# Kernel tuning notes

Measured on AMD Instinct MI355X. Metric: run time of the kernel, lower is better.

The kernel has to match this reference:

```python
import jax, jax.numpy as jnp
import numpy as np

IN_DIM = 96
HIDDEN = 256
EPS = 1e-6
NEG = -1e10


def setup_inputs() -> dict:
    key = jax.random.key(0)
    ks = jax.random.split(key, 12)
    B, S = 8, 2048
    q = jax.random.normal(ks[0], (B, S, IN_DIM), dtype=jnp.float32)
    k = jax.random.normal(ks[1], (B, S, IN_DIM), dtype=jnp.float32)
    v = jax.random.normal(ks[2], (B, S, IN_DIM), dtype=jnp.float32)
    mask = jax.random.randint(ks[3], (B, S, S), 0, 2, dtype=jnp.int32)
    s = 1.0 / np.sqrt(IN_DIM)
    Wq = jax.random.normal(ks[4], (IN_DIM, HIDDEN), dtype=jnp.float32) * s
    bq = jax.random.normal(ks[5], (HIDDEN,), dtype=jnp.float32) * 0.01
    Wk = jax.random.normal(ks[6], (IN_DIM, HIDDEN), dtype=jnp.float32) * s
    bk = jax.random.normal(ks[7], (HIDDEN,), dtype=jnp.float32) * 0.01
    Wv = jax.random.normal(ks[8], (IN_DIM, HIDDEN), dtype=jnp.float32) * s
    bv = jax.random.normal(ks[9], (HIDDEN,), dtype=jnp.float32) * 0.01
    gamma = jnp.ones((HIDDEN,), dtype=jnp.float32)
    beta = jnp.zeros((HIDDEN,), dtype=jnp.float32)
    return {"query": q, "key": k, "value": v, "mask": mask,
            "Wq": Wq, "bq": bq, "Wk": Wk, "bk": bk, "Wv": Wv, "bv": bv,
            "gamma": gamma, "beta": beta}


def reference(query, key, value, mask, Wq, bq, Wk, bk, Wv, bv, gamma, beta):
    # Linear projections: [B,S,96] @ [96,H] -> [B,S,H]
    q = jnp.einsum('bsf,fh->bsh', query, Wq) + bq
    k = jnp.einsum('bsf,fh->bsh', key, Wk) + bk
    v = jnp.einsum('bsf,fh->bsh', value, Wv) + bv
    # Scaled dot-product scores: [B,S,S]
    score = jnp.einsum('bqh,bkh->bqk', q, k) / jnp.sqrt(jnp.float32(HIDDEN))
    score = jnp.where(mask == 0, jnp.float32(NEG), score)
    attn = jax.nn.softmax(score, axis=-1)
    out = jnp.einsum('bqk,bkh->bqh', attn, v)
    # LayerNorm over last dim, eps=1e-6
    mu = jnp.mean(out, axis=-1, keepdims=True)
    var = jnp.mean(jnp.square(out - mu), axis=-1, keepdims=True)
    normed = (out - mu) * jax.lax.rsqrt(var + EPS)
    return normed * gamma + beta
```

## Files before the change

### kernel.cpp

```cpp
#include <hip/hip_runtime.h>

#define B_   8
#define S_   2048
#define IN_  96
#define H_   256
#define NROW (B_ * S_)

typedef float    f32x4 __attribute__((ext_vector_type(4)));
typedef _Float16 f16x8 __attribute__((ext_vector_type(8)));
typedef int      i32x4 __attribute__((ext_vector_type(4)));

__device__ __forceinline__ unsigned short f2h(float x) {
    return __builtin_bit_cast(unsigned short, (_Float16)x);
}
__device__ __forceinline__ float h2f(unsigned short x) {
    return (float)__builtin_bit_cast(_Float16, x);
}
__device__ __forceinline__ void lds_barrier() {
    asm volatile("s_waitcnt lgkmcnt(0)\n\ts_barrier" ::: "memory");
}

__global__ __launch_bounds__(256) void wconv_kernel(
    const float* __restrict__ Wq, const float* __restrict__ Wk,
    const float* __restrict__ Wv, unsigned short* __restrict__ wt)
{
    const int p  = blockIdx.x >> 3;
    const int h0 = (blockIdx.x & 7) * 32;
    const float* W = (p == 0) ? Wq : (p == 1) ? Wk : Wv;
    unsigned short* dst = wt + (size_t)p * H_ * IN_ + (size_t)h0 * IN_;

    __shared__ unsigned short lds[32][100];
    const int t = threadIdx.x;
    #pragma unroll
    for (int i = 0; i < 12; ++i) {
        int idx = i * 256 + t;
        int f = idx >> 5;
        int hl = idx & 31;
        lds[hl][f] = f2h(W[f * H_ + h0 + hl]);
    }
    __syncthreads();
    #pragma unroll
    for (int j = 0; j < 6; ++j) {
        int e = (j * 256 + t) * 2;
        int hl = e / IN_, f = e % IN_;
        unsigned int pk = (unsigned int)lds[hl][f] |
                          ((unsigned int)lds[hl][f + 1] << 16);
        ((unsigned int*)dst)[j * 256 + t] = pk;
    }
}

__global__ __launch_bounds__(256) void projmask_kernel(
    const float* __restrict__ query, const float* __restrict__ key,
    const float* __restrict__ value, const unsigned short* __restrict__ wt,
    const float* __restrict__ bq, const float* __restrict__ bk,
    const float* __restrict__ bv, const int* __restrict__ mask,
    unsigned short* __restrict__ pq, unsigned short* __restrict__ pk,
    unsigned short* __restrict__ pv, unsigned* __restrict__ pm32)
{
    __shared__ unsigned short Xs[3][16][104];
    __shared__ unsigned char nib[4][8][64];

    const int bid = blockIdx.x;
    if ((bid % 3) == 2) {
        const int wave = threadIdx.x >> 6;
        const int lane = threadIdx.x & 63;
        const int wid  = (bid / 3) * 4 + wave;
        #pragma unroll
        for (int rr = 0; rr < 4; ++rr) {
            const int r0 = wid * 8 + rr * 2;
            const int* m0 = mask + (size_t)r0 * S_ + lane * 4;
            const int* m1 = m0 + S_;
            i32x4 a[8], b[8];
            #pragma unroll
            for (int j = 0; j < 8; ++j)
                a[j] = __builtin_nontemporal_load((const i32x4*)(m0 + j * 256));
            #pragma unroll
            for (int j = 0; j < 8; ++j)
                b[j] = __builtin_nontemporal_load((const i32x4*)(m1 + j * 256));

            #pragma unroll
            for (int j = 0; j < 8; ++j) {
                unsigned n0 = (a[j][0] != 0 ? 1u : 0u) | (a[j][1] != 0 ? 2u : 0u)
                            | (a[j][2] != 0 ? 4u : 0u) | (a[j][3] != 0 ? 8u : 0u);
                unsigned n1 = (b[j][0] != 0 ? 1u : 0u) | (b[j][1] != 0 ? 2u : 0u)
                            | (b[j][2] != 0 ? 4u : 0u) | (b[j][3] != 0 ? 8u : 0u);
                nib[wave][j][lane] = (unsigned char)(n0 | (n1 << 4));
            }
            asm volatile("s_waitcnt lgkmcnt(0)" ::: "memory");

            unsigned long long v = *(const unsigned long long*)
                &nib[wave][lane >> 3][(lane & 7) * 8];
            unsigned long long x0 = v & 0x0F0F0F0F0F0F0F0FULL;
            unsigned long long x1 = (v >> 4) & 0x0F0F0F0F0F0F0F0FULL;
            x0 = (x0 | (x0 >> 4))  & 0x00FF00FF00FF00FFULL;
            x1 = (x1 | (x1 >> 4))  & 0x00FF00FF00FF00FFULL;
            x0 = (x0 | (x0 >> 8))  & 0x0000FFFF0000FFFFULL;
            x1 = (x1 | (x1 >> 8))  & 0x0000FFFF0000FFFFULL;
            x0 = (x0 | (x0 >> 16)) & 0xFFFFFFFFULL;
            x1 = (x1 | (x1 >> 16)) & 0xFFFFFFFFULL;

            pm32[(size_t)r0 * 64 + lane]       = (unsigned)x0;
            pm32[(size_t)(r0 + 1) * 64 + lane] = (unsigned)x1;
        }
        return;
    }
    const int bi = (bid / 3) * 2 + (bid % 3);

    const int t    = threadIdx.x;
    const int lane = t & 63;
    const int wave = t >> 6;
    const int col  = lane & 15;
    const int quad = lane >> 4;
    const int s0   = bi * 16;
    const int b    = s0 >> 11;
    const int sl   = s0 & (S_ - 1);

    const float* srcs[3] = { query + (size_t)s0 * IN_,
                             key   + (size_t)s0 * IN_,
                             value + (size_t)s0 * IN_ };
    #pragma unroll
    for (int p = 0; p < 3; ++p) {
        #pragma unroll
        for (int i = 0; i < 2; ++i) {
            int idx = i * 256 + t;
            if (idx < 384) {
                f32x4 x = *(const f32x4*)(srcs[p] + idx * 4);
                int r = idx / 24;
                int f = (idx - r * 24) * 4;
                unsigned long long pkk =
                    (unsigned long long)f2h(x[0])
                  | ((unsigned long long)f2h(x[1]) << 16)
                  | ((unsigned long long)f2h(x[2]) << 32)
                  | ((unsigned long long)f2h(x[3]) << 48);
                *(unsigned long long*)&Xs[p][r][f] = pkk;
            }
        }
    }
    __syncthreads();

    const int hc = wave;
    #pragma unroll
    for (int p = 0; p < 3; ++p) {
        const unsigned short* wbase = wt + (size_t)p * H_ * IN_;
        f16x8 wfr[4][3];
        #pragma unroll
        for (int ht = 0; ht < 4; ++ht)
            #pragma unroll
            for (int kc = 0; kc < 3; ++kc)
                wfr[ht][kc] = *(const f16x8*)(wbase
                    + (size_t)(hc * 64 + ht * 16 + col) * IN_ + kc * 32 + quad * 8);
        f16x8 xfr[3];
        #pragma unroll
        for (int kc = 0; kc < 3; ++kc)
            xfr[kc] = *(const f16x8*)&Xs[p][col][kc * 32 + quad * 8];

        f32x4 acc[4];
        #pragma unroll
        for (int ht = 0; ht < 4; ++ht) acc[ht] = (f32x4)(0.0f);
        #pragma unroll
        for (int kc = 0; kc < 3; ++kc)
            #pragma unroll
            for (int ht = 0; ht < 4; ++ht)
                acc[ht] = (p < 2)
                    ? __builtin_amdgcn_mfma_f32_16x16x32_f16(xfr[kc], wfr[ht][kc], acc[ht], 0, 0, 0)
                    : __builtin_amdgcn_mfma_f32_16x16x32_f16(wfr[ht][kc], xfr[kc], acc[ht], 0, 0, 0);

        if (p < 2) {
            unsigned short* dst  = (p == 0) ? pq : pk;
            const float*    bias = (p == 0) ? bq : bk;
            #pragma unroll
            for (int ht = 0; ht < 4; ++ht) {
                float bh = bias[hc * 64 + ht * 16 + col];
                const int s    = hc * 2 + (ht >> 1);
                const int lq   = ((ht & 1) * 2 + (col >> 3)) * 16;
                const int j    = col & 7;
                #pragma unroll
                for (int r = 0; r < 4; ++r)
                    dst[(size_t)(((bi * 8 + s) * 64 + lq + quad * 4 + r)) * 8 + j]
                        = f2h(acc[ht][r] + bh);
            }
        } else {
            const int kl  = (sl & 63) + col;
            const int c   = sl >> 6;
            const int s2  = kl >> 5;
            const int qv  = (kl >> 3) & 3;
            const int jj  = col & 7;
            #pragma unroll
            for (int ht = 0; ht < 4; ++ht) {
                f32x4 b4 = *(const f32x4*)(bv + hc * 64 + ht * 16 + quad * 4);
                #pragma unroll
                for (int r = 0; r < 4; ++r)
                    pv[(size_t)(((b * 32 + c) * 32 + hc * 8 + ht * 2 + s2) * 64
                                + qv * 16 + quad * 4 + r) * 8 + jj]
                        = f2h(acc[ht][r] + b4[r]);
            }
        }
    }
}

__global__ __launch_bounds__(256, 3) void attn_kernel(
    const unsigned short* __restrict__ pq, const unsigned short* __restrict__ pk,
    const unsigned short* __restrict__ pv, const unsigned long long* __restrict__ pm,
    const float* __restrict__ gamma, const float* __restrict__ beta,
    float* __restrict__ out)
{
    __shared__ __align__(16) unsigned short Qs[8448];
    __shared__ unsigned short P[2][32][68];
    __shared__ float lsum[4][32];
    __shared__ float linv_s[32];

    const int tid  = threadIdx.x;
    const int wave = tid >> 6;
    const int lane = tid & 63;
    const int col  = lane & 15;
    const int quad = lane >> 4;

    const int b     = blockIdx.x & 7;
    const int strip = blockIdx.x >> 3;
    const int q0    = strip << 5;

    {
        const unsigned short* qsrc = pq + (size_t)(b * 128 + strip * 2) * 4096;
        #pragma unroll
        for (int ph = 0; ph < 4; ++ph) {
            int i = ph * 2048 + tid * 8;
            *(f16x8*)&Qs[i] = *(const f16x8*)(qsrc + i);
        }
    }

    f32x4 O[2][4];
    #pragma unroll
    for (int st = 0; st < 2; ++st)
        #pragma unroll
        for (int ht = 0; ht < 4; ++ht) O[st][ht] = (f32x4)(0.0f);
    float l0 = 0.0f, l1 = 0.0f;

    const unsigned short* pkb = pk + (size_t)(b * 128) * 4096 + lane * 8;
    const unsigned short* pvb = pv + (size_t)(b * 32) * 32 * 512
                                   + (size_t)wave * 8 * 512 + lane * 8;

    const unsigned* pm32 = (const unsigned*)pm;
    const int sh = (wave & 1) * 16 + quad * 4;
    const unsigned* mp0 = pm32 + (size_t)(b * S_ + q0 + col) * 64 + (wave >> 1);
    const unsigned* mp1 = mp0 + 16 * 64;

    f16x8 kf[8];
    #pragma unroll
    for (int s = 0; s < 8; ++s)
        kf[s] = *(const f16x8*)(pkb + (size_t)wave * 4096 + s * 512);

    unsigned mc0 = mp0[0];
    unsigned mc1 = mp1[0];

    lds_barrier();

    {
        f32x4 St0 = (f32x4)(0.0f), St1 = (f32x4)(0.0f);
        __builtin_amdgcn_s_setprio(1);
        #pragma unroll
        for (int s = 0; s < 8; ++s) {
            f16x8 q0f = *(const f16x8*)&Qs[s * 512 + lane * 8];
            f16x8 q1f = *(const f16x8*)&Qs[4096 + s * 512 + lane * 8];
            St0 = __builtin_amdgcn_mfma_f32_16x16x32_f16(kf[s], q0f, St0, 0, 0, 0);
            St1 = __builtin_amdgcn_mfma_f32_16x16x32_f16(kf[s], q1f, St1, 0, 0, 0);
        }
        __builtin_amdgcn_s_setprio(0);

        {
            const unsigned short* kb = pkb + (size_t)(4 + wave) * 4096;
            #pragma unroll
            for (int s = 0; s < 8; ++s)
                kf[s] = *(const f16x8*)(kb + s * 512);
        }
        unsigned mn0 = mp0[2];
        unsigned mn1 = mp1[2];

        {
            unsigned bits = mc0 >> sh;
            unsigned long long pk64 = 0;
            #pragma unroll
            for (int r = 0; r < 4; ++r) {
                float e = exp2f(fmaf(St0[r], 0.0901679843f, -8.65617025f));
                float p = ((bits >> r) & 1u) ? e : 0.0f;
                _Float16 ph = (_Float16)p;
                l0 += (float)ph;
                pk64 |= (unsigned long long)__builtin_bit_cast(unsigned short, ph)
                        << (16 * r);
            }
            *(unsigned long long*)&P[0][col][wave * 16 + quad * 4] = pk64;
        }
        {
            unsigned bits = mc1 >> sh;
            unsigned long long pk64 = 0;
            #pragma unroll
            for (int r = 0; r < 4; ++r) {
                float e = exp2f(fmaf(St1[r], 0.0901679843f, -8.65617025f));
                float p = ((bits >> r) & 1u) ? e : 0.0f;
                _Float16 ph = (_Float16)p;
                l1 += (float)ph;
                pk64 |= (unsigned long long)__builtin_bit_cast(unsigned short, ph)
                        << (16 * r);
            }
            *(unsigned long long*)&P[0][16 + col][wave * 16 + quad * 4] = pk64;
        }
        mc0 = mn0; mc1 = mn1;

        lds_barrier();
    }

    #pragma unroll 2
    for (int i = 0; i < 31; ++i) {
        const int pb  = i & 1;
        const int cn2 = (i < 29) ? i + 2 : 31;

        const unsigned short* vb = pvb + (size_t)i * 32 * 512;
        f16x8 vf[4][2];
        #pragma unroll
        for (int ht = 0; ht < 4; ++ht)
            #pragma unroll
            for (int s2 = 0; s2 < 2; ++s2)
                vf[ht][s2] = *(const f16x8*)(vb + (size_t)(ht * 2 + s2) * 512);

        f32x4 St0 = (f32x4)(0.0f), St1 = (f32x4)(0.0f);
        __builtin_amdgcn_s_setprio(1);
        #pragma unroll
        for (int s = 0; s < 8; ++s) {
            f16x8 q0f = *(const f16x8*)&Qs[s * 512 + lane * 8];
            f16x8 q1f = *(const f16x8*)&Qs[4096 + s * 512 + lane * 8];
            St0 = __builtin_amdgcn_mfma_f32_16x16x32_f16(kf[s], q0f, St0, 0, 0, 0);
            St1 = __builtin_amdgcn_mfma_f32_16x16x32_f16(kf[s], q1f, St1, 0, 0, 0);
        }
        __builtin_amdgcn_s_setprio(0);

        {
            const unsigned short* kb = pkb + (size_t)(cn2 * 4 + wave) * 4096;
            #pragma unroll
            for (int s = 0; s < 8; ++s)
                kf[s] = *(const f16x8*)(kb + s * 512);
        }
        unsigned mn0 = mp0[cn2 * 2];
        unsigned mn1 = mp1[cn2 * 2];

        {
            unsigned bits = mc0 >> sh;
            unsigned long long pk64 = 0;
            #pragma unroll
            for (int r = 0; r < 4; ++r) {
                float e = exp2f(fmaf(St0[r], 0.0901679843f, -8.65617025f));
                float p = ((bits >> r) & 1u) ? e : 0.0f;
                _Float16 ph = (_Float16)p;
                l0 += (float)ph;
                pk64 |= (unsigned long long)__builtin_bit_cast(unsigned short, ph)
                        << (16 * r);
            }
            *(unsigned long long*)&P[pb ^ 1][col][wave * 16 + quad * 4] = pk64;
        }
        {
            unsigned bits = mc1 >> sh;
            unsigned long long pk64 = 0;
            #pragma unroll
            for (int r = 0; r < 4; ++r) {
                float e = exp2f(fmaf(St1[r], 0.0901679843f, -8.65617025f));
                float p = ((bits >> r) & 1u) ? e : 0.0f;
                _Float16 ph = (_Float16)p;
                l1 += (float)ph;
                pk64 |= (unsigned long long)__builtin_bit_cast(unsigned short, ph)
                        << (16 * r);
            }
            *(unsigned long long*)&P[pb ^ 1][16 + col][wave * 16 + quad * 4] = pk64;
        }
        mc0 = mn0; mc1 = mn1;

        __builtin_amdgcn_s_setprio(1);
        #pragma unroll
        for (int st = 0; st < 2; ++st) {
            #pragma unroll
            for (int s2 = 0; s2 < 2; ++s2) {
                union { unsigned long long u[2]; f16x8 v; } pu;
                const unsigned short* pr = &P[pb][st * 16 + col][s2 * 32 + quad * 8];
                pu.u[0] = *(const unsigned long long*)pr;
                pu.u[1] = *(const unsigned long long*)(pr + 4);
                f16x8 pf = pu.v;
                #pragma unroll
                for (int ht = 0; ht < 4; ++ht)
                    O[st][ht] = __builtin_amdgcn_mfma_f32_16x16x32_f16(pf, vf[ht][s2], O[st][ht], 0, 0, 0);
            }
        }
        __builtin_amdgcn_s_setprio(0);

        lds_barrier();
    }

    {
        const unsigned short* vb = pvb + (size_t)31 * 32 * 512;
        f16x8 vf[4][2];
        #pragma unroll
        for (int ht = 0; ht < 4; ++ht)
            #pragma unroll
            for (int s2 = 0; s2 < 2; ++s2)
                vf[ht][s2] = *(const f16x8*)(vb + (size_t)(ht * 2 + s2) * 512);
        __builtin_amdgcn_s_setprio(1);
        #pragma unroll
        for (int st = 0; st < 2; ++st) {
            #pragma unroll
            for (int s2 = 0; s2 < 2; ++s2) {
                union { unsigned long long u[2]; f16x8 v; } pu;
                const unsigned short* pr = &P[1][st * 16 + col][s2 * 32 + quad * 8];
                pu.u[0] = *(const unsigned long long*)pr;
                pu.u[1] = *(const unsigned long long*)(pr + 4);
                f16x8 pf = pu.v;
                #pragma unroll
                for (int ht = 0; ht < 4; ++ht)
                    O[st][ht] = __builtin_amdgcn_mfma_f32_16x16x32_f16(pf, vf[ht][s2], O[st][ht], 0, 0, 0);
            }
        }
        __builtin_amdgcn_s_setprio(0);
    }

    l0 += __shfl_xor(l0, 16); l0 += __shfl_xor(l0, 32);
    l1 += __shfl_xor(l1, 16); l1 += __shfl_xor(l1, 32);
    if (lane < 16) { lsum[wave][lane] = l0; lsum[wave][16 + lane] = l1; }
    __syncthreads();

    if (tid < 32) {
        float lt = lsum[0][tid] + lsum[1][tid] + lsum[2][tid] + lsum[3][tid];
        linv_s[tid] = 1.0f / lt;
    }

    unsigned short* OT = Qs;
    #pragma unroll
    for (int st = 0; st < 2; ++st)
        #pragma unroll
        for (int ht = 0; ht < 4; ++ht)
            #pragma unroll
            for (int r = 0; r < 4; ++r)
                OT[(st * 16 + quad * 4 + r) * 264 + wave * 64 + ht * 16 + col]
                    = f2h(O[st][ht][r]);
    __syncthreads();

    f32x4 g  = *(const f32x4*)(gamma + lane * 4);
    f32x4 be = *(const f32x4*)(beta  + lane * 4);
    #pragma unroll
    for (int p = 0; p < 8; ++p) {
        const int row = p * 4 + wave;
        float linv = linv_s[row];
        unsigned long long a =
            *(const unsigned long long*)&OT[row * 264 + lane * 4];
        float vals[4];
        float sum = 0.0f;
        #pragma unroll
        for (int j = 0; j < 4; ++j) {
            vals[j] = h2f((unsigned short)(a >> (16 * j))) * linv;
            sum += vals[j];
        }
        sum += __shfl_xor(sum, 1);  sum += __shfl_xor(sum, 2);
        sum += __shfl_xor(sum, 4);  sum += __shfl_xor(sum, 8);
        sum += __shfl_xor(sum, 16); sum += __shfl_xor(sum, 32);
        float mu = sum * (1.0f / H_);

        float sq = 0.0f;
        #pragma unroll
        for (int j = 0; j < 4; ++j) {
            float d = vals[j] - mu;
            sq += d * d;
        }
        sq += __shfl_xor(sq, 1);  sq += __shfl_xor(sq, 2);
        sq += __shfl_xor(sq, 4);  sq += __shfl_xor(sq, 8);
        sq += __shfl_xor(sq, 16); sq += __shfl_xor(sq, 32);
        float rstd = rsqrtf(sq * (1.0f / H_) + 1e-6f);

        f32x4 o;
        #pragma unroll
        for (int j = 0; j < 4; ++j)
            o[j] = (vals[j] - mu) * rstd * g[j] + be[j];
        *(f32x4*)(out + (size_t)(b * S_ + q0 + row) * H_ + lane * 4) = o;
    }
}

extern "C" void kernel_launch(void* const* d_in, const int* in_sizes, int n_in,
                              void* d_out, int out_size, void* d_ws, size_t ws_size,
                              hipStream_t stream)
{
    const float* query = (const float*)d_in[0];
    const float* key   = (const float*)d_in[1];
    const float* value = (const float*)d_in[2];
    const int*   mask  = (const int*)d_in[3];
    const float* Wq = (const float*)d_in[4];
    const float* bq = (const float*)d_in[5];
    const float* Wk = (const float*)d_in[6];
    const float* bk = (const float*)d_in[7];
    const float* Wv = (const float*)d_in[8];
    const float* bv = (const float*)d_in[9];
    const float* gamma = (const float*)d_in[10];
    const float* beta  = (const float*)d_in[11];
    float* out = (float*)d_out;

    const size_t NQK = (size_t)B_ * S_ * H_;
    unsigned short* pq = (unsigned short*)d_ws;
    unsigned short* pk = pq + NQK;
    unsigned short* pv = pk + NQK;
    unsigned short* wt = pv + NQK;
    unsigned long long* pm = (unsigned long long*)
        (wt + (size_t)3 * H_ * IN_);

    wconv_kernel<<<24, 256, 0, stream>>>(Wq, Wk, Wv, wt);
    projmask_kernel<<<1536, 256, 0, stream>>>(query, key, value, wt,
                                              bq, bk, bv, mask,
                                              pq, pk, pv, (unsigned*)pm);
    attn_kernel<<<512, 256, 0, stream>>>(pq, pk, pv, pm, gamma, beta, out);
}
```

Baseline: 291.5 us.

## Keep softmax probabilities in registers and split keys across waves with cross-wave O reduction

Each wave now owns a distinct 16-key slice per iteration and feeds its exp'd scores directly as the A operand of 16x16x16 MFMAs against a full-H V tile, removing the LDS P buffer and per-iteration barriers. The V projection output layout is rewritten to match the new fragment order. Each wave accumulates a full 32x256 partial O (128 accumulator registers), which is reduced across the four waves through an fp32 LDS scratch at the end. The cost is much higher register pressure (launch bounds lowered to 2 blocks), more LDS, a larger epilogue reduction, and use of the smaller-K MFMA instruction.

```diff
diff --git a/kernel.cpp b/kernel.cpp
--- a/kernel.cpp
+++ b/kernel.cpp
@@ -8,6 +8,7 @@
 
 typedef float    f32x4 __attribute__((ext_vector_type(4)));
 typedef _Float16 f16x8 __attribute__((ext_vector_type(8)));
+typedef _Float16 f16x4 __attribute__((ext_vector_type(4)));
 typedef int      i32x4 __attribute__((ext_vector_type(4)));
 
 __device__ __forceinline__ unsigned short f2h(float x) {
@@ -180,32 +181,33 @@
                         = f2h(acc[ht][r] + bh);
             }
         } else {
-            const int kl  = (sl & 63) + col;
-            const int c   = sl >> 6;
-            const int s2  = kl >> 5;
-            const int qv  = (kl >> 3) & 3;
-            const int jj  = col & 7;
+            const int c16 = sl >> 4;
+            const int qd  = col >> 2;
+            const int jj  = col & 3;
             #pragma unroll
             for (int ht = 0; ht < 4; ++ht) {
+                const int htp = hc * 4 + ht;
                 f32x4 b4 = *(const f32x4*)(bv + hc * 64 + ht * 16 + quad * 4);
                 #pragma unroll
-                for (int r = 0; r < 4; ++r)
-                    pv[(size_t)(((b * 32 + c) * 32 + hc * 8 + ht * 2 + s2) * 64
-                                + qv * 16 + quad * 4 + r) * 8 + jj]
+                for (int r = 0; r < 4; ++r) {
+                    const int lanep = qd * 16 + quad * 4 + r;
+                    pv[(size_t)((b * 128 + c16) * 8 + (htp >> 1)) * 512
+                       + lanep * 8 + (htp & 1) * 4 + jj]
                         = f2h(acc[ht][r] + b4[r]);
-            }
-        }
-    }
-}
-
-__global__ __launch_bounds__(256, 3) void attn_kernel(
+                }
+            }
+        }
+    }
+}
+
+__global__ __launch_bounds__(256, 2) void attn_kernel(
     const unsigned short* __restrict__ pq, const unsigned short* __restrict__ pk,
     const unsigned short* __restrict__ pv, const unsigned long long* __restrict__ pm,
     const float* __restrict__ gamma, const float* __restrict__ beta,
     float* __restrict__ out)
 {
     __shared__ __align__(16) unsigned short Qs[8448];
-    __shared__ unsigned short P[2][32][68];
+    __shared__ __align__(16) float scratch[4][32][68];
     __shared__ float lsum[4][32];
     __shared__ float linv_s[32];
 
@@ -228,16 +230,15 @@
         }
     }
 
-    f32x4 O[2][4];
+    f32x4 O[2][16];
     #pragma unroll
     for (int st = 0; st < 2; ++st)
         #pragma unroll
-        for (int ht = 0; ht < 4; ++ht) O[st][ht] = (f32x4)(0.0f);
+        for (int t2 = 0; t2 < 16; ++t2) O[st][t2] = (f32x4)(0.0f);
     float l0 = 0.0f, l1 = 0.0f;
 
     const unsigned short* pkb = pk + (size_t)(b * 128) * 4096 + lane * 8;
-    const unsigned short* pvb = pv + (size_t)(b * 32) * 32 * 512
-                                   + (size_t)wave * 8 * 512 + lane * 8;
+    const unsigned short* pvb = pv + (size_t)(b * 128) * 4096 + lane * 8;
 
     const unsigned* pm32 = (const unsigned*)pm;
     const int sh = (wave & 1) * 16 + quad * 4;
@@ -254,7 +255,14 @@
 
     lds_barrier();
 
-    {
+    for (int i = 0; i < 32; ++i) {
+        const size_t c16 = (size_t)(i * 4 + wave);
+
+        f16x8 vf[8];
+        #pragma unroll
+        for (int t2 = 0; t2 < 8; ++t2)
+            vf[t2] = *(const f16x8*)(pvb + c16 * 4096 + t2 * 512);
+
         f32x4 St0 = (f32x4)(0.0f), St1 = (f32x4)(0.0f);
         __builtin_amdgcn_s_setprio(1);
         #pragma unroll
@@ -267,152 +275,51 @@
         __builtin_amdgcn_s_setprio(0);
 
         {
-            const unsigned short* kb = pkb + (size_t)(4 + wave) * 4096;
+            const size_t cn = (i < 31) ? c16 + 4 : c16;
             #pragma unroll
             for (int s = 0; s < 8; ++s)
-                kf[s] = *(const f16x8*)(kb + s * 512);
-        }
-        unsigned mn0 = mp0[2];
-        unsigned mn1 = mp1[2];
-
+                kf[s] = *(const f16x8*)(pkb + cn * 4096 + s * 512);
+        }
+        unsigned mn0 = mp0[(size_t)((i < 31 ? i + 1 : i) * 2)];
+        unsigned mn1 = mp1[(size_t)((i < 31 ? i + 1 : i) * 2)];
+
+        f16x4 pf0, pf1;
         {
             unsigned bits = mc0 >> sh;
-            unsigned long long pk64 = 0;
             #pragma unroll
             for (int r = 0; r < 4; ++r) {
                 float e = exp2f(fmaf(St0[r], 0.0901679843f, -8.65617025f));
                 float p = ((bits >> r) & 1u) ? e : 0.0f;
                 _Float16 ph = (_Float16)p;
                 l0 += (float)ph;
-                pk64 |= (unsigned long long)__builtin_bit_cast(unsigned short, ph)
-                        << (16 * r);
-            }
-            *(unsigned long long*)&P[0][col][wave * 16 + quad * 4] = pk64;
+                pf0[r] = ph;
+            }
         }
         {
             unsigned bits = mc1 >> sh;
-            unsigned long long pk64 = 0;
             #pragma unroll
             for (int r = 0; r < 4; ++r) {
                 float e = exp2f(fmaf(St1[r], 0.0901679843f, -8.65617025f));
                 float p = ((bits >> r) & 1u) ? e : 0.0f;
                 _Float16 ph = (_Float16)p;
                 l1 += (float)ph;
-                pk64 |= (unsigned long long)__builtin_bit_cast(unsigned short, ph)
-                        << (16 * r);
-            }
-            *(unsigned long long*)&P[0][16 + col][wave * 16 + quad * 4] = pk64;
+                pf1[r] = ph;
+            }
         }
         mc0 = mn0; mc1 = mn1;
 
-        lds_barrier();
-    }
-
-    #pragma unroll 2
-    for (int i = 0; i < 31; ++i) {
-        const int pb  = i & 1;
-        const int cn2 = (i < 29) ? i + 2 : 31;
-
-        const unsigned short* vb = pvb + (size_t)i * 32 * 512;
-        f16x8 vf[4][2];
-        #pragma unroll
-        for (int ht = 0; ht < 4; ++ht)
-            #pragma unroll
-            for (int s2 = 0; s2 < 2; ++s2)
-                vf[ht][s2] = *(const f16x8*)(vb + (size_t)(ht * 2 + s2) * 512);
-
-        f32x4 St0 = (f32x4)(0.0f), St1 = (f32x4)(0.0f);
         __builtin_amdgcn_s_setprio(1);
         #pragma unroll
-        for (int s = 0; s < 8; ++s) {
-            f16x8 q0f = *(const f16x8*)&Qs[s * 512 + lane * 8];
-            f16x8 q1f = *(const f16x8*)&Qs[4096 + s * 512 + lane * 8];
-            St0 = __builtin_amdgcn_mfma_f32_16x16x32_f16(kf[s], q0f, St0, 0, 0, 0);
-            St1 = __builtin_amdgcn_mfma_f32_16x16x32_f16(kf[s], q1f, St1, 0, 0, 0);
-        }
-        __builtin_amdgcn_s_setprio(0);
-
-        {
-            const unsigned short* kb = pkb + (size_t)(cn2 * 4 + wave) * 4096;
-            #pragma unroll
-            for (int s = 0; s < 8; ++s)
-                kf[s] = *(const f16x8*)(kb + s * 512);
-        }
-        unsigned mn0 = mp0[cn2 * 2];
-        unsigned mn1 = mp1[cn2 * 2];
-
-        {
-            unsigned bits = mc0 >> sh;
-            unsigned long long pk64 = 0;
-            #pragma unroll
-            for (int r = 0; r < 4; ++r) {
-                float e = exp2f(fmaf(St0[r], 0.0901679843f, -8.65617025f));
-                float p = ((bits >> r) & 1u) ? e : 0.0f;
-                _Float16 ph = (_Float16)p;
-                l0 += (float)ph;
-                pk64 |= (unsigned long long)__builtin_bit_cast(unsigned short, ph)
-                        << (16 * r);
-            }
-            *(unsigned long long*)&P[pb ^ 1][col][wave * 16 + quad * 4] = pk64;
-        }
-        {
-            unsigned bits = mc1 >> sh;
-            unsigned long long pk64 = 0;
-            #pragma unroll
-            for (int r = 0; r < 4; ++r) {
-                float e = exp2f(fmaf(St1[r], 0.0901679843f, -8.65617025f));
-                float p = ((bits >> r) & 1u) ? e : 0.0f;
-                _Float16 ph = (_Float16)p;
-                l1 += (float)ph;
-                pk64 |= (unsigned long long)__builtin_bit_cast(unsigned short, ph)
-                        << (16 * r);
-            }
-            *(unsigned long long*)&P[pb ^ 1][16 + col][wave * 16 + quad * 4] = pk64;
-        }
-        mc0 = mn0; mc1 = mn1;
-
-        __builtin_amdgcn_s_setprio(1);
-        #pragma unroll
-        for (int st = 0; st < 2; ++st) {
-            #pragma unroll
-            for (int s2 = 0; s2 < 2; ++s2) {
-                union { unsigned long long u[2]; f16x8 v; } pu;
-                const unsigned short* pr = &P[pb][st * 16 + col][s2 * 32 + quad * 8];
-                pu.u[0] = *(const unsigned long long*)pr;
-                pu.u[1] = *(const unsigned long long*)(pr + 4);
-                f16x8 pf = pu.v;
-                #pragma unroll
-                for (int ht = 0; ht < 4; ++ht)
-                    O[st][ht] = __builtin_amdgcn_mfma_f32_16x16x32_f16(pf, vf[ht][s2], O[st][ht], 0, 0, 0);
-            }
-        }
-        __builtin_amdgcn_s_setprio(0);
-
-        lds_barrier();
-    }
-
-    {
-        const unsigned short* vb = pvb + (size_t)31 * 32 * 512;
-        f16x8 vf[4][2];
-        #pragma unroll
-        for (int ht = 0; ht < 4; ++ht)
-            #pragma unroll
-            for (int s2 = 0; s2 < 2; ++s2)
-                vf[ht][s2] = *(const f16x8*)(vb + (size_t)(ht * 2 + s2) * 512);
-        __builtin_amdgcn_s_setprio(1);
-        #pragma unroll
-        for (int st = 0; st < 2; ++st) {
-            #pragma unroll
-            for (int s2 = 0; s2 < 2; ++s2) {
-                union { unsigned long long u[2]; f16x8 v; } pu;
-                const unsigned short* pr = &P[1][st * 16 + col][s2 * 32 + quad * 8];
-                pu.u[0] = *(const unsigned long long*)pr;
-                pu.u[1] = *(const unsigned long long*)(pr + 4);
-                f16x8 pf = pu.v;
-                #pragma unroll
-                for (int ht = 0; ht < 4; ++ht)
-                    O[st][ht] = __builtin_amdgcn_mfma_f32_16x16x32_f16(pf, vf[ht][s2], O[st][ht], 0, 0, 0);
-            }
+        for (int t2 = 0; t2 < 8; ++t2) {
+            f16x4 blo, bhi;
+            blo[0] = vf[t2][0]; blo[1] = vf[t2][1];
+            blo[2] = vf[t2][2]; blo[3] = vf[t2][3];
+            bhi[0] = vf[t2][4]; bhi[1] = vf[t2][5];
+            bhi[2] = vf[t2][6]; bhi[3] = vf[t2][7];
+            O[0][t2 * 2]     = __builtin_amdgcn_mfma_f32_16x16x16f16(pf0, blo, O[0][t2 * 2],     0, 0, 0);
+            O[0][t2 * 2 + 1] = __builtin_amdgcn_mfma_f32_16x16x16f16(pf0, bhi, O[0][t2 * 2 + 1], 0, 0, 0);
+            O[1][t2 * 2]     = __builtin_amdgcn_mfma_f32_16x16x16f16(pf1, blo, O[1][t2 * 2],     0, 0, 0);
+            O[1][t2 * 2 + 1] = __builtin_amdgcn_mfma_f32_16x16x16f16(pf1, bhi, O[1][t2 * 2 + 1], 0, 0, 0);
         }
         __builtin_amdgcn_s_setprio(0);
     }
@@ -429,14 +336,41 @@
 
     unsigned short* OT = Qs;
     #pragma unroll
-    for (int st = 0; st < 2; ++st)
-        #pragma unroll
-        for (int ht = 0; ht < 4; ++ht)
-            #pragma unroll
-            for (int r = 0; r < 4; ++r)
-                OT[(st * 16 + quad * 4 + r) * 264 + wave * 64 + ht * 16 + col]
-                    = f2h(O[st][ht][r]);
-    __syncthreads();
+    for (int hr = 0; hr < 4; ++hr) {
+        #pragma unroll
+        for (int st = 0; st < 2; ++st)
+            #pragma unroll
+            for (int k = 0; k < 4; ++k)
+                #pragma unroll
+                for (int r = 0; r < 4; ++r)
+                    scratch[wave][st * 16 + quad * 4 + r][k * 16 + col]
+                        = O[st][hr * 4 + k][r];
+        __syncthreads();
+        {
+            const int q = tid >> 3, j = tid & 7;
+            f32x4 alo = *(const f32x4*)&scratch[0][q][j * 8];
+            f32x4 ahi = *(const f32x4*)&scratch[0][q][j * 8 + 4];
+            #pragma unroll
+            for (int w = 1; w < 4; ++w) {
+                alo += *(const f32x4*)&scratch[w][q][j * 8];
+                ahi += *(const f32x4*)&scratch[w][q][j * 8 + 4];
+            }
+            unsigned long long w0 =
+                  (unsigned long long)f2h(alo[0])
+                | ((unsigned long long)f2h(alo[1]) << 16)
+                | ((unsigned long long)f2h(alo[2]) << 32)
+                | ((unsigned long long)f2h(alo[3]) << 48);
+            unsigned long long w1 =
+                  (unsigned long long)f2h(ahi[0])
+                | ((unsigned long long)f2h(ahi[1]) << 16)
+                | ((unsigned long long)f2h(ahi[2]) << 32)
+                | ((unsigned long long)f2h(ahi[3]) << 48);
+            unsigned short* ot = &OT[q * 264 + hr * 64 + j * 8];
+            *(unsigned long long*)ot       = w0;
+            *(unsigned long long*)(ot + 4) = w1;
+        }
+        __syncthreads();
+    }
 
     f32x4 g  = *(const f32x4*)(gamma + lane * 4);
     f32x4 be = *(const f32x4*)(beta  + lane * 4);
```

New measurement: 462.6 us. 1.59x slower.
